# Kernel tuning notes

Hardware: AMD Instinct MI355X
Metric: run time of the kernel (lower is better)

Reference implementation:

```python
import jax, jax.numpy as jnp
import numpy as np

B, N, H, W = 128, 8192, 7, 7


def setup_inputs() -> dict:
    key = jax.random.key(0)
    ks = jax.random.split(key, 10)
    inp = {
        'x': jax.random.normal(ks[0], (B, N, H, W), dtype=jnp.float32),
        'y': jax.random.normal(ks[1], (B, N), dtype=jnp.float32),
        # nn.MultiheadAttention(embed_dim=1, num_heads=1) params (all scalar)
        'wq': jax.random.normal(ks[2], (), dtype=jnp.float32),
        'wk': jax.random.normal(ks[3], (), dtype=jnp.float32),
        'wv': jax.random.normal(ks[4], (), dtype=jnp.float32),
        'bq': jax.random.normal(ks[5], (), dtype=jnp.float32) * 0.1,
        'bk': jax.random.normal(ks[6], (), dtype=jnp.float32) * 0.1,
        'bv': jax.random.normal(ks[7], (), dtype=jnp.float32) * 0.1,
        'wo': jax.random.normal(ks[8], (), dtype=jnp.float32),
        'bo': jax.random.normal(ks[9], (), dtype=jnp.float32) * 0.1,
    }
    return inp


def _mha1(q_src, kv_src, wq, bq, wk, bk, wv, bv, wo, bo):
    # embed_dim=1, num_heads=1, scale = 1/sqrt(1) = 1.
    # torch sees (seq=B, batch=N, embed=1): attention mixes the B axis per n.
    q = q_src * wq + bq            # [B, N]
    k = kv_src * wk + bk           # [B, N]
    v = kv_src * wv + bv           # [B, N]
    scores = jnp.einsum('in,jn->ijn', q, k)      # [B, B, N]
    a = jax.nn.softmax(scores, axis=1)           # softmax over keys j
    out = jnp.einsum('ijn,jn->in', a, v)         # [B, N]
    return out * wo + bo


def reference(x, y, wq, bq, wk, bk, wv, bv, wo, bo):
    xp = jnp.mean(x, axis=(2, 3))                # AdaptiveAvgPool2d((1,1)) -> [B, N]
    self_x = _mha1(xp, xp, wq, bq, wk, bk, wv, bv, wo, bo)
    self_y = _mha1(y, y, wq, bq, wk, bk, wv, bv, wo, bo)
    cross_x = _mha1(xp, y, wq, bq, wk, bk, wv, bv, wo, bo)
    cross_y = _mha1(y, xp, wq, bq, wk, bk, wv, bv, wo, bo)
    f_x = xp + self_x
    f_y = y + self_y
    c_f_x = cross_x + f_x
    c_f_y = cross_y + f_y
    return jnp.concatenate((c_f_x, c_f_y), axis=1)   # [B, 2N]
```

## Files before the change

kernel.cpp:

```cpp
#include <hip/hip_runtime.h>


constexpr int B_SEQ = 128;
constexpr int N_COL = 8192;
constexpr int HWP   = 49;
constexpr int NT    = 256;
constexpr int TC    = 4;
constexpr int G     = 4;
constexpr int CPB   = TC * G;
constexpr int VSTR  = 132;
constexpr int OSTR  = 21;

typedef float v2f __attribute__((ext_vector_type(2)));

#if __has_builtin(__builtin_elementwise_fma)
#define VFMA(a, b, c) __builtin_elementwise_fma((a), (b), (c))
#else
__device__ __forceinline__ v2f VFMA(v2f a, v2f b, v2f c) {
    v2f r; r.x = fmaf(a.x, b.x, c.x); r.y = fmaf(a.y, b.y, c.y); return r;
}
#endif

__global__ __launch_bounds__(NT, 2) void rsca_fused(
    const float* __restrict__ x, const float* __restrict__ y,
    const float* __restrict__ pwq, const float* __restrict__ pwk,
    const float* __restrict__ pwv, const float* __restrict__ pbq,
    const float* __restrict__ pbk, const float* __restrict__ pbv,
    const float* __restrict__ pwo, const float* __restrict__ pbo,
    float* __restrict__ out)
{
    __shared__ float vls[2][2][TC * VSTR];
    __shared__ float pmn[2][2][8][TC];
    __shared__ float pmx[2][2][8][TC];
    __shared__ float obuf[2][B_SEQ * OSTR];

    const int t       = threadIdx.x;
    const int bid     = blockIdx.x;
    const int colbase = bid * CPB;
    const int ql      = t & 3;
    const int seg     = t >> 2;
    const int lane    = t & 63;
    const int wid     = t >> 6;

    const float wq = pwq[0], wk = pwk[0], wv = pwv[0];
    const float bq = pbq[0], bk = pbk[0], bv = pbv[0];
    const float wo = pwo[0], bo = pbo[0];
    const float L2E = 1.4426950408889634f;
    const float wkL = wk * L2E, bkL = bk * L2E;
    const float alpha = wo * wv;
    const float beta2 = 2.0f * (wo * bv + bo);

    auto issue_pass = [&](int g, int p, float4 (&v)[13]) {
        const int j = p * 64 + seg;
        const float4* __restrict__ base =
            (const float4*)(x + ((size_t)j * N_COL + colbase + g * TC) * (size_t)HWP);
        #pragma unroll
        for (int k = 0; k < 12; ++k) v[k] = base[ql + 4 * k];
        v[12] = base[48];
    };

    auto reduce_pass = [&](int p, int nb, const float4 (&v)[13]) {
        float s0 = 0.f, s1 = 0.f, s2 = 0.f, s3 = 0.f;
        s0 += v[0].x + v[0].y + v[0].z + v[0].w;
        s0 += v[1].x + v[1].y + v[1].z + v[1].w;
        s0 += v[2].x + v[2].y + v[2].z + v[2].w;
        s1 += v[4].x + v[4].y + v[4].z + v[4].w;
        s1 += v[5].x + v[5].y + v[5].z + v[5].w;
        s2 += v[7].x + v[7].y + v[7].z + v[7].w;
        s2 += v[8].x + v[8].y + v[8].z + v[8].w;
        s3 += v[10].x + v[10].y + v[10].z + v[10].w;
        s3 += v[11].x + v[11].y + v[11].z + v[11].w;
        { const float sm = v[3].x + v[3].y + v[3].z + v[3].w;
          const float cr = (ql == 0) ? v[3].x : 0.0f;
          s0 += cr; s1 += sm - cr; }
        { const float sm = v[6].x + v[6].y + v[6].z + v[6].w;
          const float cr = (ql == 0) ? (v[6].x + v[6].y) : 0.0f;
          s1 += cr; s2 += sm - cr; }
        { const float sm = v[9].x + v[9].y + v[9].z + v[9].w;
          const float cr = (ql == 0) ? (v[9].x + v[9].y + v[9].z) : 0.0f;
          s2 += cr; s3 += sm - cr; }
        const float tail = v[12].x + v[12].y + v[12].z + v[12].w;
        s0 += __shfl_xor(s0, 1); s1 += __shfl_xor(s1, 1);
        s2 += __shfl_xor(s2, 1); s3 += __shfl_xor(s3, 1);
        s0 += __shfl_xor(s0, 2); s1 += __shfl_xor(s1, 2);
        s2 += __shfl_xor(s2, 2); s3 += __shfl_xor(s3, 2);
        float r = s0;
        r = (ql == 1) ? s1 : r;
        r = (ql == 2) ? s2 : r;
        r = (ql == 3) ? (s3 + tail) : r;
        const float mean = r * (1.0f / HWP);
        const int j = p * 64 + seg;
        vls[nb][0][ql * VSTR + j] = mean;
        float mn = mean, mx = mean;
        #pragma unroll
        for (int off = 4; off <= 32; off <<= 1) {
            mn = fminf(mn, __shfl_xor(mn, off));
            mx = fmaxf(mx, __shfl_xor(mx, off));
        }
        if (lane < 4) {
            pmn[nb][0][p * 4 + wid][ql] = mn;
            pmx[nb][0][p * 4 + wid][ql] = mx;
        }
    };

    auto stage_y = [&](int nb, float fy0, float fy1) {
        vls[nb][1][ql * VSTR + seg]      = fy0;
        vls[nb][1][ql * VSTR + seg + 64] = fy1;
        float mn = fminf(fy0, fy1), mx = fmaxf(fy0, fy1);
        #pragma unroll
        for (int off = 4; off <= 32; off <<= 1) {
            mn = fminf(mn, __shfl_xor(mn, off));
            mx = fmaxf(mx, __shfl_xor(mx, off));
        }
        if (lane < 4) {
            pmn[nb][1][wid][ql] = mn;
            pmx[nb][1][wid][ql] = mx;
        }
    };

    const int ch = t >> 7;
    const int i  = t & (B_SEQ - 1);

    auto attn = [&](int g, int cb, int cc) {
        const int c = ch * 2 + cc;
        const float* __restrict__ vx = &vls[cb][0][c * VSTR];
        const float* __restrict__ vy = &vls[cb][1][c * VSTR];

        float vxmn = pmn[cb][0][0][c], vxmx = pmx[cb][0][0][c];
        #pragma unroll
        for (int s = 1; s < 8; ++s) {
            vxmn = fminf(vxmn, pmn[cb][0][s][c]);
            vxmx = fmaxf(vxmx, pmx[cb][0][s][c]);
        }
        float vymn = pmn[cb][1][0][c], vymx = pmx[cb][1][0][c];
        #pragma unroll
        for (int s = 1; s < 4; ++s) {
            vymn = fminf(vymn, pmn[cb][1][s][c]);
            vymx = fmaxf(vymx, pmx[cb][1][s][c]);
        }
        const float axv = fmaf(vxmx, wkL, bkL), bxv = fmaf(vxmn, wkL, bkL);
        const float kxmx = fmaxf(axv, bxv), kxmn = fminf(axv, bxv);
        const float ayv = fmaf(vymx, wkL, bkL), byv = fmaf(vymn, wkL, bkL);
        const float kymx = fmaxf(ayv, byv), kymn = fminf(ayv, byv);

        const float xi = vx[i], yi = vy[i];
        const float qx = fmaf(xi, wq, bq), qy = fmaf(yi, wq, bq);
        const float nmsx = -(qx >= 0.f ? qx * kxmx : qx * kxmn);
        const float nmcy = -(qy >= 0.f ? qy * kxmx : qy * kxmn);
        const float nmsy = -(qy >= 0.f ? qy * kymx : qy * kymn);
        const float nmcx = -(qx >= 0.f ? qx * kymx : qx * kymn);

        const float qxw = qx * wkL, qyw = qy * wkL;
        const v2f qxw2 = {qxw, qxw}, qyw2 = {qyw, qyw};
        const float csx = fmaf(qx, bkL, nmsx), ccy = fmaf(qy, bkL, nmcy);
        const float csy = fmaf(qy, bkL, nmsy), ccx = fmaf(qx, bkL, nmcx);
        const v2f csx2 = {csx, csx}, ccy2 = {ccy, ccy};
        const v2f csy2 = {csy, csy}, ccx2 = {ccx, ccx};

        v2f s0sx = {0.f, 0.f}, s1sx = {0.f, 0.f};
        v2f s0cy = {0.f, 0.f}, s1cy = {0.f, 0.f};
        v2f s0sy = {0.f, 0.f}, s1sy = {0.f, 0.f};
        v2f s0cx = {0.f, 0.f}, s1cx = {0.f, 0.f};

        for (int j0 = 0; j0 < B_SEQ; j0 += 8) {
            const float4 a0 = *(const float4*)&vx[j0];
            const float4 a1 = *(const float4*)&vx[j0 + 4];
            const float4 b0 = *(const float4*)&vy[j0];
            const float4 b1 = *(const float4*)&vy[j0 + 4];
            auto px2 = [&](float v0, float v1) {
                const v2f vv = {v0, v1};
                v2f t1 = VFMA(qxw2, vv, csx2);
                v2f e1; e1.x = __builtin_amdgcn_exp2f(t1.x);
                        e1.y = __builtin_amdgcn_exp2f(t1.y);
                s1sx = VFMA(e1, vv, s1sx); s0sx += e1;
                v2f t2 = VFMA(qyw2, vv, ccy2);
                v2f e2; e2.x = __builtin_amdgcn_exp2f(t2.x);
                        e2.y = __builtin_amdgcn_exp2f(t2.y);
                s1cy = VFMA(e2, vv, s1cy); s0cy += e2;
            };
            auto py2 = [&](float v0, float v1) {
                const v2f vv = {v0, v1};
                v2f t3 = VFMA(qyw2, vv, csy2);
                v2f e3; e3.x = __builtin_amdgcn_exp2f(t3.x);
                        e3.y = __builtin_amdgcn_exp2f(t3.y);
                s1sy = VFMA(e3, vv, s1sy); s0sy += e3;
                v2f t4 = VFMA(qxw2, vv, ccx2);
                v2f e4; e4.x = __builtin_amdgcn_exp2f(t4.x);
                        e4.y = __builtin_amdgcn_exp2f(t4.y);
                s1cx = VFMA(e4, vv, s1cx); s0cx += e4;
            };
            px2(a0.x, a0.y); px2(a0.z, a0.w); px2(a1.x, a1.y); px2(a1.z, a1.w);
            py2(b0.x, b0.y); py2(b0.z, b0.w); py2(b1.x, b1.y); py2(b1.z, b1.w);
        }
        const float S0sx = s0sx.x + s0sx.y, S1sx = s1sx.x + s1sx.y;
        const float S0cy = s0cy.x + s0cy.y, S1cy = s1cy.x + s1cy.y;
        const float S0sy = s0sy.x + s0sy.y, S1sy = s1sy.x + s1sy.y;
        const float S0cx = s0cx.x + s0cx.y, S1cx = s1cx.x + s1cx.y;
        const float mx_attn = S1sx * __builtin_amdgcn_rcpf(S0sx)
                            + S1cx * __builtin_amdgcn_rcpf(S0cx);
        const float my_attn = S1sy * __builtin_amdgcn_rcpf(S0sy)
                            + S1cy * __builtin_amdgcn_rcpf(S0cy);
        obuf[0][i * OSTR + g * TC + c] = fmaf(alpha, mx_attn, beta2 + xi);
        obuf[1][i * OSTR + g * TC + c] = fmaf(alpha, my_attn, beta2 + yi);
    };

    float4 va[13], vb[13];
    float fy0, fy1;
    {
        const int col = colbase + ql;
        issue_pass(0, 0, va);
        issue_pass(0, 1, vb);
        fy0 = y[(size_t)seg * N_COL + col];
        fy1 = y[(size_t)(seg + 64) * N_COL + col];
        reduce_pass(0, 0, va);
        stage_y(0, fy0, fy1);
        reduce_pass(1, 0, vb);
    }
    __syncthreads();

    int cur = 0;
    for (int g = 0; g < G; ++g) {
        const int nb = cur ^ 1;
        const bool pf = (g + 1 < G);
        if (pf) {
            const int col = colbase + (g + 1) * TC + ql;
            issue_pass(g + 1, 0, va);
            fy0 = y[(size_t)seg * N_COL + col];
            fy1 = y[(size_t)(seg + 64) * N_COL + col];
        }
        attn(g, cur, 0);
        if (pf) {
            reduce_pass(0, nb, va);
            stage_y(nb, fy0, fy1);
            issue_pass(g + 1, 1, vb);
        }
        attn(g, cur, 1);
        if (pf) reduce_pass(1, nb, vb);
        __syncthreads();
        cur = nb;
    }

    #pragma unroll
    for (int idx = t; idx < 2 * B_SEQ * TC; idx += NT) {
        const int set = idx >> 9;
        const int rem = idx & 511;
        const int ii  = rem >> 2;
        const int q   = rem & 3;
        const float* p = &obuf[set][ii * OSTR + q * 4];
        float4 val;
        val.x = p[0]; val.y = p[1]; val.z = p[2]; val.w = p[3];
        *(float4*)&out[(size_t)ii * (2 * N_COL) + (size_t)set * N_COL + colbase + q * 4] = val;
    }
}

extern "C" void kernel_launch(void* const* d_in, const int* in_sizes, int n_in,
                              void* d_out, int out_size, void* d_ws, size_t ws_size,
                              hipStream_t stream) {
    const float* x   = (const float*)d_in[0];
    const float* y   = (const float*)d_in[1];
    const float* pwq = (const float*)d_in[2];
    const float* pwk = (const float*)d_in[3];
    const float* pwv = (const float*)d_in[4];
    const float* pbq = (const float*)d_in[5];
    const float* pbk = (const float*)d_in[6];
    const float* pbv = (const float*)d_in[7];
    const float* pwo = (const float*)d_in[8];
    const float* pbo = (const float*)d_in[9];
    float* out = (float*)d_out;

    rsca_fused<<<dim3(N_COL / CPB), dim3(NT), 0, stream>>>(
        x, y, pwq, pwk, pwv, pbq, pbk, pbv, pwo, pbo, out);
}
```

Before: 326.5 us.

## Split fused kernel into pooling pass and separate attention kernel via workspace

Replaces the single fused pool+attention kernel with two kernels when a workspace is available. The first pools x into a transposed [N,B] buffer, and the second runs the attention with 512-thread blocks over 16 columns and a swizzled block-to-column mapping. The aim is to let the memory-bound pooling and the exp-bound attention each run with their own occupancy instead of being interleaved in one kernel. The cost is an extra global round trip for the pooled values and a second launch. The old fused path stays as a fallback when no workspace is given.

```diff
diff --git a/kernel.cpp b/kernel.cpp
--- a/kernel.cpp
+++ b/kernel.cpp
@@ -4,12 +4,6 @@
 constexpr int B_SEQ = 128;
 constexpr int N_COL = 8192;
 constexpr int HWP   = 49;
-constexpr int NT    = 256;
-constexpr int TC    = 4;
-constexpr int G     = 4;
-constexpr int CPB   = TC * G;
-constexpr int VSTR  = 132;
-constexpr int OSTR  = 21;
 
 typedef float v2f __attribute__((ext_vector_type(2)));
 
@@ -20,6 +14,227 @@
     v2f r; r.x = fmaf(a.x, b.x, c.x); r.y = fmaf(a.y, b.y, c.y); return r;
 }
 #endif
+
+constexpr int ANT = 256;
+constexpr int ATC = 4;
+
+__global__ __launch_bounds__(ANT, 6) void pool_x(
+    const float* __restrict__ x, float* __restrict__ xpT)
+{
+    const int t   = threadIdx.x;
+    const int n0  = blockIdx.x * ATC;
+    const int ql  = t & 3;
+    const int seg = t >> 2;
+
+    for (int pass = 0; pass < 2; ++pass) {
+        const int j = pass * 64 + seg;
+        const float4* __restrict__ base =
+            (const float4*)(x + ((size_t)j * N_COL + n0) * (size_t)HWP);
+        float4 v[13];
+        #pragma unroll
+        for (int k = 0; k < 12; ++k) v[k] = base[ql + 4 * k];
+        v[12] = base[48];
+
+        float s0 = 0.f, s1 = 0.f, s2 = 0.f, s3 = 0.f;
+        s0 += v[0].x + v[0].y + v[0].z + v[0].w;
+        s0 += v[1].x + v[1].y + v[1].z + v[1].w;
+        s0 += v[2].x + v[2].y + v[2].z + v[2].w;
+        s1 += v[4].x + v[4].y + v[4].z + v[4].w;
+        s1 += v[5].x + v[5].y + v[5].z + v[5].w;
+        s2 += v[7].x + v[7].y + v[7].z + v[7].w;
+        s2 += v[8].x + v[8].y + v[8].z + v[8].w;
+        s3 += v[10].x + v[10].y + v[10].z + v[10].w;
+        s3 += v[11].x + v[11].y + v[11].z + v[11].w;
+        { const float sm = v[3].x + v[3].y + v[3].z + v[3].w;
+          const float cr = (ql == 0) ? v[3].x : 0.0f;
+          s0 += cr; s1 += sm - cr; }
+        { const float sm = v[6].x + v[6].y + v[6].z + v[6].w;
+          const float cr = (ql == 0) ? (v[6].x + v[6].y) : 0.0f;
+          s1 += cr; s2 += sm - cr; }
+        { const float sm = v[9].x + v[9].y + v[9].z + v[9].w;
+          const float cr = (ql == 0) ? (v[9].x + v[9].y + v[9].z) : 0.0f;
+          s2 += cr; s3 += sm - cr; }
+        const float tail = v[12].x + v[12].y + v[12].z + v[12].w;
+
+        s0 += __shfl_xor(s0, 1); s1 += __shfl_xor(s1, 1);
+        s2 += __shfl_xor(s2, 1); s3 += __shfl_xor(s3, 1);
+        s0 += __shfl_xor(s0, 2); s1 += __shfl_xor(s1, 2);
+        s2 += __shfl_xor(s2, 2); s3 += __shfl_xor(s3, 2);
+        float r = s0;
+        r = (ql == 1) ? s1 : r;
+        r = (ql == 2) ? s2 : r;
+        r = (ql == 3) ? (s3 + tail) : r;
+        const float mean = r * (1.0f / HWP);
+        xpT[(size_t)(n0 + ql) * B_SEQ + j] = mean;
+    }
+}
+
+constexpr int BNT = 512;
+constexpr int BTC = 16;
+constexpr int OPAD = 17;
+
+__global__ __launch_bounds__(BNT, 4) void rsca_attn(
+    const float* __restrict__ xpT, const float* __restrict__ y,
+    const float* __restrict__ pwq, const float* __restrict__ pwk,
+    const float* __restrict__ pwv, const float* __restrict__ pbq,
+    const float* __restrict__ pbk, const float* __restrict__ pbv,
+    const float* __restrict__ pwo, const float* __restrict__ pbo,
+    float* __restrict__ out)
+{
+    __shared__ float xv[BTC][B_SEQ];
+    __shared__ float yv[BTC][B_SEQ];
+    __shared__ float pmny[8][BTC], pmxy[8][BTC];
+    __shared__ float pmnx[BTC], pmxx[BTC];
+    __shared__ float obuf[2][B_SEQ * OPAD];
+
+    const int t    = threadIdx.x;
+    const int lane = t & 63;
+    const int wv   = t >> 6;
+    const int cg = (blockIdx.x & 7) * ((int)gridDim.x >> 3) + (blockIdx.x >> 3);
+    const int n0 = cg * BTC;
+
+    const float wq = pwq[0], wk = pwk[0], wvv = pwv[0];
+    const float bq = pbq[0], bk = pbk[0], bv = pbv[0];
+    const float wo = pwo[0], bo = pbo[0];
+    const float L2E = 1.4426950408889634f;
+    const float wkL = wk * L2E, bkL = bk * L2E;
+    const float alpha = wo * wvv;
+    const float beta2 = 2.0f * (wo * bv + bo);
+
+    {
+        const float4 v4 = *(const float4*)&xpT[(size_t)n0 * B_SEQ + t * 4];
+        const int c  = t >> 5;
+        const int j0 = (t & 31) * 4;
+        *(float4*)&xv[c][j0] = v4;
+        float mn = fminf(fminf(v4.x, v4.y), fminf(v4.z, v4.w));
+        float mx = fmaxf(fmaxf(v4.x, v4.y), fmaxf(v4.z, v4.w));
+        #pragma unroll
+        for (int off = 1; off <= 16; off <<= 1) {
+            mn = fminf(mn, __shfl_xor(mn, off));
+            mx = fmaxf(mx, __shfl_xor(mx, off));
+        }
+        if ((lane & 31) == 0) { pmnx[c] = mn; pmxx[c] = mx; }
+    }
+    {
+        const int c  = t & 15;
+        const int jb = t >> 4;
+        float fy[4];
+        #pragma unroll
+        for (int r = 0; r < 4; ++r)
+            fy[r] = y[(size_t)(jb + 32 * r) * N_COL + n0 + c];
+        #pragma unroll
+        for (int r = 0; r < 4; ++r)
+            yv[c][jb + 32 * r] = fy[r];
+        float mn = fminf(fminf(fy[0], fy[1]), fminf(fy[2], fy[3]));
+        float mx = fmaxf(fmaxf(fy[0], fy[1]), fmaxf(fy[2], fy[3]));
+        mn = fminf(mn, __shfl_xor(mn, 16)); mx = fmaxf(mx, __shfl_xor(mx, 16));
+        mn = fminf(mn, __shfl_xor(mn, 32)); mx = fmaxf(mx, __shfl_xor(mx, 32));
+        if (lane < 16) { pmny[wv][c] = mn; pmxy[wv][c] = mx; }
+    }
+    __syncthreads();
+
+    const int ch = t >> 7;
+    const int i  = t & (B_SEQ - 1);
+
+    #pragma unroll
+    for (int cc = 0; cc < 4; ++cc) {
+        const int c = ch * 4 + cc;
+        const float* __restrict__ vx = xv[c];
+        const float* __restrict__ vy = yv[c];
+
+        const float vxmn = pmnx[c], vxmx = pmxx[c];
+        float vymn = pmny[0][c], vymx = pmxy[0][c];
+        #pragma unroll
+        for (int s = 1; s < 8; ++s) {
+            vymn = fminf(vymn, pmny[s][c]);
+            vymx = fmaxf(vymx, pmxy[s][c]);
+        }
+        const float axv = fmaf(vxmx, wkL, bkL), bxv = fmaf(vxmn, wkL, bkL);
+        const float kxmx = fmaxf(axv, bxv), kxmn = fminf(axv, bxv);
+        const float ayv = fmaf(vymx, wkL, bkL), byv = fmaf(vymn, wkL, bkL);
+        const float kymx = fmaxf(ayv, byv), kymn = fminf(ayv, byv);
+
+        const float xi = vx[i], yi = vy[i];
+        const float qx = fmaf(xi, wq, bq), qy = fmaf(yi, wq, bq);
+        const float nmsx = -(qx >= 0.f ? qx * kxmx : qx * kxmn);
+        const float nmcy = -(qy >= 0.f ? qy * kxmx : qy * kxmn);
+        const float nmsy = -(qy >= 0.f ? qy * kymx : qy * kymn);
+        const float nmcx = -(qx >= 0.f ? qx * kymx : qx * kymn);
+
+        const float qxw = qx * wkL, qyw = qy * wkL;
+        const v2f qxw2 = {qxw, qxw}, qyw2 = {qyw, qyw};
+        const float csx = fmaf(qx, bkL, nmsx), ccy = fmaf(qy, bkL, nmcy);
+        const float csy = fmaf(qy, bkL, nmsy), ccx = fmaf(qx, bkL, nmcx);
+        const v2f csx2 = {csx, csx}, ccy2 = {ccy, ccy};
+        const v2f csy2 = {csy, csy}, ccx2 = {ccx, ccx};
+
+        v2f s0sx = {0.f, 0.f}, s1sx = {0.f, 0.f};
+        v2f s0cy = {0.f, 0.f}, s1cy = {0.f, 0.f};
+        v2f s0sy = {0.f, 0.f}, s1sy = {0.f, 0.f};
+        v2f s0cx = {0.f, 0.f}, s1cx = {0.f, 0.f};
+
+        for (int j0 = 0; j0 < B_SEQ; j0 += 8) {
+            const float4 a0 = *(const float4*)&vx[j0];
+            const float4 a1 = *(const float4*)&vx[j0 + 4];
+            const float4 b0 = *(const float4*)&vy[j0];
+            const float4 b1 = *(const float4*)&vy[j0 + 4];
+            auto px2 = [&](float v0, float v1) {
+                const v2f vvj = {v0, v1};
+                v2f t1 = VFMA(qxw2, vvj, csx2);
+                v2f e1; e1.x = __builtin_amdgcn_exp2f(t1.x);
+                        e1.y = __builtin_amdgcn_exp2f(t1.y);
+                s1sx = VFMA(e1, vvj, s1sx); s0sx += e1;
+                v2f t2 = VFMA(qyw2, vvj, ccy2);
+                v2f e2; e2.x = __builtin_amdgcn_exp2f(t2.x);
+                        e2.y = __builtin_amdgcn_exp2f(t2.y);
+                s1cy = VFMA(e2, vvj, s1cy); s0cy += e2;
+            };
+            auto py2 = [&](float v0, float v1) {
+                const v2f vvj = {v0, v1};
+                v2f t3 = VFMA(qyw2, vvj, csy2);
+                v2f e3; e3.x = __builtin_amdgcn_exp2f(t3.x);
+                        e3.y = __builtin_amdgcn_exp2f(t3.y);
+                s1sy = VFMA(e3, vvj, s1sy); s0sy += e3;
+                v2f t4 = VFMA(qxw2, vvj, ccx2);
+                v2f e4; e4.x = __builtin_amdgcn_exp2f(t4.x);
+                        e4.y = __builtin_amdgcn_exp2f(t4.y);
+                s1cx = VFMA(e4, vvj, s1cx); s0cx += e4;
+            };
+            px2(a0.x, a0.y); px2(a0.z, a0.w); px2(a1.x, a1.y); px2(a1.z, a1.w);
+            py2(b0.x, b0.y); py2(b0.z, b0.w); py2(b1.x, b1.y); py2(b1.z, b1.w);
+        }
+        const float S0sx = s0sx.x + s0sx.y, S1sx = s1sx.x + s1sx.y;
+        const float S0cy = s0cy.x + s0cy.y, S1cy = s1cy.x + s1cy.y;
+        const float S0sy = s0sy.x + s0sy.y, S1sy = s1sy.x + s1sy.y;
+        const float S0cx = s0cx.x + s0cx.y, S1cx = s1cx.x + s1cx.y;
+        const float mx_attn = S1sx * __builtin_amdgcn_rcpf(S0sx)
+                            + S1cx * __builtin_amdgcn_rcpf(S0cx);
+        const float my_attn = S1sy * __builtin_amdgcn_rcpf(S0sy)
+                            + S1cy * __builtin_amdgcn_rcpf(S0cy);
+        obuf[0][i * OPAD + c] = fmaf(alpha, mx_attn, beta2 + xi);
+        obuf[1][i * OPAD + c] = fmaf(alpha, my_attn, beta2 + yi);
+    }
+    __syncthreads();
+
+    #pragma unroll
+    for (int k = 0; k < 2; ++k) {
+        const int fidx = t + k * BNT;
+        const int q   = fidx & 3;
+        const int ii  = (fidx >> 2) & (B_SEQ - 1);
+        const int set = fidx >> 9;
+        const float* p = &obuf[set][ii * OPAD + q * 4];
+        float4 val;
+        val.x = p[0]; val.y = p[1]; val.z = p[2]; val.w = p[3];
+        *(float4*)&out[(size_t)ii * (2 * N_COL) + (size_t)set * N_COL + n0 + q * 4] = val;
+    }
+}
+
+constexpr int NT  = 256;
+constexpr int TC  = 4;
+constexpr int G   = 4;
+constexpr int CPB = TC * G;
+constexpr int VSTR = 132;
+constexpr int OSTR = 21;
 
 __global__ __launch_bounds__(NT, 2) void rsca_fused(
     const float* __restrict__ x, const float* __restrict__ y,
@@ -123,8 +338,8 @@
 
     auto attn = [&](int g, int cb, int cc) {
         const int c = ch * 2 + cc;
-        const float* __restrict__ vx = &vls[cb][0][c * VSTR];
-        const float* __restrict__ vy = &vls[cb][1][c * VSTR];
+        const float* __restrict__ vx0 = &vls[cb][0][c * VSTR];
+        const float* __restrict__ vy0 = &vls[cb][1][c * VSTR];
 
         float vxmn = pmn[cb][0][0][c], vxmx = pmx[cb][0][0][c];
         #pragma unroll
@@ -143,7 +358,7 @@
         const float ayv = fmaf(vymx, wkL, bkL), byv = fmaf(vymn, wkL, bkL);
         const float kymx = fmaxf(ayv, byv), kymn = fminf(ayv, byv);
 
-        const float xi = vx[i], yi = vy[i];
+        const float xi = vx0[i], yi = vy0[i];
         const float qx = fmaf(xi, wq, bq), qy = fmaf(yi, wq, bq);
         const float nmsx = -(qx >= 0.f ? qx * kxmx : qx * kxmn);
         const float nmcy = -(qy >= 0.f ? qy * kxmx : qy * kxmn);
@@ -163,10 +378,10 @@
         v2f s0cx = {0.f, 0.f}, s1cx = {0.f, 0.f};
 
         for (int j0 = 0; j0 < B_SEQ; j0 += 8) {
-            const float4 a0 = *(const float4*)&vx[j0];
-            const float4 a1 = *(const float4*)&vx[j0 + 4];
-            const float4 b0 = *(const float4*)&vy[j0];
-            const float4 b1 = *(const float4*)&vy[j0 + 4];
+            const float4 a0 = *(const float4*)&vx0[j0];
+            const float4 a1 = *(const float4*)&vx0[j0 + 4];
+            const float4 b0 = *(const float4*)&vy0[j0];
+            const float4 b1 = *(const float4*)&vy0[j0 + 4];
             auto px2 = [&](float v0, float v1) {
                 const v2f vv = {v0, v1};
                 v2f t1 = VFMA(qxw2, vv, csx2);
@@ -268,6 +483,14 @@
     const float* pbo = (const float*)d_in[9];
     float* out = (float*)d_out;
 
-    rsca_fused<<<dim3(N_COL / CPB), dim3(NT), 0, stream>>>(
-        x, y, pwq, pwk, pwv, pbq, pbk, pbv, pwo, pbo, out);
+    const size_t need = (size_t)N_COL * B_SEQ * sizeof(float);
+    if (d_ws != nullptr && ws_size >= need) {
+        float* xpT = (float*)d_ws;
+        pool_x<<<dim3(N_COL / ATC), dim3(ANT), 0, stream>>>(x, xpT);
+        rsca_attn<<<dim3(N_COL / BTC), dim3(BNT), 0, stream>>>(
+            xpT, y, pwq, pwk, pwv, pbq, pbk, pbv, pwo, pbo, out);
+    } else {
+        rsca_fused<<<dim3(N_COL / CPB), dim3(NT), 0, stream>>>(
+            x, y, pwq, pwk, pwv, pbq, pbk, pbv, pwo, pbo, out);
+    }
 }
```

Measured after the change: 365.1 us. +11.8%, slower.

## Replace in-block double-buffered column groups with one 4-column group per block

Applied to the files above, without the earlier changes.

Each block now handles only 4 columns instead of 16, which removes the software-pipelined double-buffer loop and launches four times as many blocks. Launch bounds are raised to ask for more resident blocks per CU, and the blocks are remapped with an XCD-style swizzle of the block index. The attention inner loop also prefetches the next 8 shared-memory values one iteration ahead. The intent is to rely on occupancy across blocks rather than manual overlap to hide load latency. The cost is narrower output stores, extra per-block setup, and a tighter register budget.

```diff
diff --git a/kernel.cpp b/kernel.cpp
--- a/kernel.cpp
+++ b/kernel.cpp
@@ -6,10 +6,8 @@
 constexpr int HWP   = 49;
 constexpr int NT    = 256;
 constexpr int TC    = 4;
-constexpr int G     = 4;
-constexpr int CPB   = TC * G;
 constexpr int VSTR  = 132;
-constexpr int OSTR  = 21;
+constexpr int OSTR  = 5;
 
 typedef float v2f __attribute__((ext_vector_type(2)));
 
@@ -21,7 +19,7 @@
 }
 #endif
 
-__global__ __launch_bounds__(NT, 2) void rsca_fused(
+__global__ __launch_bounds__(NT, 5) void rsca_fused(
     const float* __restrict__ x, const float* __restrict__ y,
     const float* __restrict__ pwq, const float* __restrict__ pwk,
     const float* __restrict__ pwv, const float* __restrict__ pbq,
@@ -29,18 +27,21 @@
     const float* __restrict__ pwo, const float* __restrict__ pbo,
     float* __restrict__ out)
 {
-    __shared__ float vls[2][2][TC * VSTR];
-    __shared__ float pmn[2][2][8][TC];
-    __shared__ float pmx[2][2][8][TC];
+    __shared__ float xv[TC * VSTR];
+    __shared__ float yv[TC * VSTR];
+    __shared__ float pmnx[8][TC], pmxx[8][TC];
+    __shared__ float pmny[4][TC], pmxy[4][TC];
     __shared__ float obuf[2][B_SEQ * OSTR];
 
-    const int t       = threadIdx.x;
-    const int bid     = blockIdx.x;
-    const int colbase = bid * CPB;
-    const int ql      = t & 3;
-    const int seg     = t >> 2;
-    const int lane    = t & 63;
-    const int wid     = t >> 6;
+    const int t    = threadIdx.x;
+    const int bid  = blockIdx.x;
+    const int cg = (bid & 7) * ((N_COL / TC) >> 3) + (bid >> 3);
+    const int n0 = cg * TC;
+
+    const int ql   = t & 3;
+    const int seg  = t >> 2;
+    const int lane = t & 63;
+    const int wid  = t >> 6;
 
     const float wq = pwq[0], wk = pwk[0], wv = pwv[0];
     const float bq = pbq[0], bk = pbk[0], bv = pbv[0];
@@ -50,16 +51,30 @@
     const float alpha = wo * wv;
     const float beta2 = 2.0f * (wo * bv + bo);
 
-    auto issue_pass = [&](int g, int p, float4 (&v)[13]) {
-        const int j = p * 64 + seg;
+    {
+        const int j = t >> 2, c = t & 3;
+        const float fy0 = y[(size_t)j * N_COL + n0 + c];
+        const float fy1 = y[(size_t)(j + 64) * N_COL + n0 + c];
+        yv[c * VSTR + j]      = fy0;
+        yv[c * VSTR + j + 64] = fy1;
+        float mn = fminf(fy0, fy1), mx = fmaxf(fy0, fy1);
+        #pragma unroll
+        for (int off = 4; off <= 32; off <<= 1) {
+            mn = fminf(mn, __shfl_xor(mn, off));
+            mx = fmaxf(mx, __shfl_xor(mx, off));
+        }
+        if (lane < 4) { pmny[wid][lane] = mn; pmxy[wid][lane] = mx; }
+    }
+
+    for (int pass = 0; pass < 2; ++pass) {
+        const int j = pass * 64 + seg;
         const float4* __restrict__ base =
-            (const float4*)(x + ((size_t)j * N_COL + colbase + g * TC) * (size_t)HWP);
+            (const float4*)(x + ((size_t)j * N_COL + n0) * (size_t)HWP);
+        float4 v[13];
         #pragma unroll
         for (int k = 0; k < 12; ++k) v[k] = base[ql + 4 * k];
         v[12] = base[48];
-    };
-
-    auto reduce_pass = [&](int p, int nb, const float4 (&v)[13]) {
+
         float s0 = 0.f, s1 = 0.f, s2 = 0.f, s3 = 0.f;
         s0 += v[0].x + v[0].y + v[0].z + v[0].w;
         s0 += v[1].x + v[1].y + v[1].z + v[1].w;
@@ -80,6 +95,7 @@
           const float cr = (ql == 0) ? (v[9].x + v[9].y + v[9].z) : 0.0f;
           s2 += cr; s3 += sm - cr; }
         const float tail = v[12].x + v[12].y + v[12].z + v[12].w;
+
         s0 += __shfl_xor(s0, 1); s1 += __shfl_xor(s1, 1);
         s2 += __shfl_xor(s2, 1); s3 += __shfl_xor(s3, 1);
         s0 += __shfl_xor(s0, 2); s1 += __shfl_xor(s1, 2);
@@ -89,8 +105,8 @@
         r = (ql == 2) ? s2 : r;
         r = (ql == 3) ? (s3 + tail) : r;
         const float mean = r * (1.0f / HWP);
-        const int j = p * 64 + seg;
-        vls[nb][0][ql * VSTR + j] = mean;
+        xv[ql * VSTR + j] = mean;
+
         float mn = mean, mx = mean;
         #pragma unroll
         for (int off = 4; off <= 32; off <<= 1) {
@@ -98,45 +114,31 @@
             mx = fmaxf(mx, __shfl_xor(mx, off));
         }
         if (lane < 4) {
-            pmn[nb][0][p * 4 + wid][ql] = mn;
-            pmx[nb][0][p * 4 + wid][ql] = mx;
-        }
-    };
-
-    auto stage_y = [&](int nb, float fy0, float fy1) {
-        vls[nb][1][ql * VSTR + seg]      = fy0;
-        vls[nb][1][ql * VSTR + seg + 64] = fy1;
-        float mn = fminf(fy0, fy1), mx = fmaxf(fy0, fy1);
-        #pragma unroll
-        for (int off = 4; off <= 32; off <<= 1) {
-            mn = fminf(mn, __shfl_xor(mn, off));
-            mx = fmaxf(mx, __shfl_xor(mx, off));
-        }
-        if (lane < 4) {
-            pmn[nb][1][wid][ql] = mn;
-            pmx[nb][1][wid][ql] = mx;
-        }
-    };
-
+            pmnx[pass * 4 + wid][lane] = mn;
+            pmxx[pass * 4 + wid][lane] = mx;
+        }
+    }
+    __syncthreads();
+
+    const int i  = t & (B_SEQ - 1);
     const int ch = t >> 7;
-    const int i  = t & (B_SEQ - 1);
-
-    auto attn = [&](int g, int cb, int cc) {
+    #pragma unroll
+    for (int cc = 0; cc < 2; ++cc) {
         const int c = ch * 2 + cc;
-        const float* __restrict__ vx = &vls[cb][0][c * VSTR];
-        const float* __restrict__ vy = &vls[cb][1][c * VSTR];
-
-        float vxmn = pmn[cb][0][0][c], vxmx = pmx[cb][0][0][c];
+        const float* __restrict__ vx = &xv[c * VSTR];
+        const float* __restrict__ vy = &yv[c * VSTR];
+
+        float vxmn = pmnx[0][c], vxmx = pmxx[0][c];
         #pragma unroll
         for (int s = 1; s < 8; ++s) {
-            vxmn = fminf(vxmn, pmn[cb][0][s][c]);
-            vxmx = fmaxf(vxmx, pmx[cb][0][s][c]);
-        }
-        float vymn = pmn[cb][1][0][c], vymx = pmx[cb][1][0][c];
+            vxmn = fminf(vxmn, pmnx[s][c]);
+            vxmx = fmaxf(vxmx, pmxx[s][c]);
+        }
+        float vymn = pmny[0][c], vymx = pmxy[0][c];
         #pragma unroll
         for (int s = 1; s < 4; ++s) {
-            vymn = fminf(vymn, pmn[cb][1][s][c]);
-            vymx = fmaxf(vymx, pmx[cb][1][s][c]);
+            vymn = fminf(vymn, pmny[s][c]);
+            vymx = fmaxf(vymx, pmxy[s][c]);
         }
         const float axv = fmaf(vxmx, wkL, bkL), bxv = fmaf(vxmn, wkL, bkL);
         const float kxmx = fmaxf(axv, bxv), kxmn = fminf(axv, bxv);
@@ -162,35 +164,42 @@
         v2f s0sy = {0.f, 0.f}, s1sy = {0.f, 0.f};
         v2f s0cx = {0.f, 0.f}, s1cx = {0.f, 0.f};
 
+        auto px2 = [&](float v0, float v1) {
+            const v2f vvj = {v0, v1};
+            v2f t1 = VFMA(qxw2, vvj, csx2);
+            v2f e1; e1.x = __builtin_amdgcn_exp2f(t1.x);
+                    e1.y = __builtin_amdgcn_exp2f(t1.y);
+            s1sx = VFMA(e1, vvj, s1sx); s0sx += e1;
+            v2f t2 = VFMA(qyw2, vvj, ccy2);
+            v2f e2; e2.x = __builtin_amdgcn_exp2f(t2.x);
+                    e2.y = __builtin_amdgcn_exp2f(t2.y);
+            s1cy = VFMA(e2, vvj, s1cy); s0cy += e2;
+        };
+        auto py2 = [&](float v0, float v1) {
+            const v2f vvj = {v0, v1};
+            v2f t3 = VFMA(qyw2, vvj, csy2);
+            v2f e3; e3.x = __builtin_amdgcn_exp2f(t3.x);
+                    e3.y = __builtin_amdgcn_exp2f(t3.y);
+            s1sy = VFMA(e3, vvj, s1sy); s0sy += e3;
+            v2f t4 = VFMA(qxw2, vvj, ccx2);
+            v2f e4; e4.x = __builtin_amdgcn_exp2f(t4.x);
+                    e4.y = __builtin_amdgcn_exp2f(t4.y);
+            s1cx = VFMA(e4, vvj, s1cx); s0cx += e4;
+        };
+
+        float4 a0 = *(const float4*)&vx[0], a1 = *(const float4*)&vx[4];
+        float4 b0 = *(const float4*)&vy[0], b1 = *(const float4*)&vy[4];
         for (int j0 = 0; j0 < B_SEQ; j0 += 8) {
-            const float4 a0 = *(const float4*)&vx[j0];
-            const float4 a1 = *(const float4*)&vx[j0 + 4];
-            const float4 b0 = *(const float4*)&vy[j0];
-            const float4 b1 = *(const float4*)&vy[j0 + 4];
-            auto px2 = [&](float v0, float v1) {
-                const v2f vv = {v0, v1};
-                v2f t1 = VFMA(qxw2, vv, csx2);
-                v2f e1; e1.x = __builtin_amdgcn_exp2f(t1.x);
-                        e1.y = __builtin_amdgcn_exp2f(t1.y);
-                s1sx = VFMA(e1, vv, s1sx); s0sx += e1;
-                v2f t2 = VFMA(qyw2, vv, ccy2);
-                v2f e2; e2.x = __builtin_amdgcn_exp2f(t2.x);
-                        e2.y = __builtin_amdgcn_exp2f(t2.y);
-                s1cy = VFMA(e2, vv, s1cy); s0cy += e2;
-            };
-            auto py2 = [&](float v0, float v1) {
-                const v2f vv = {v0, v1};
-                v2f t3 = VFMA(qyw2, vv, csy2);
-                v2f e3; e3.x = __builtin_amdgcn_exp2f(t3.x);
-                        e3.y = __builtin_amdgcn_exp2f(t3.y);
-                s1sy = VFMA(e3, vv, s1sy); s0sy += e3;
-                v2f t4 = VFMA(qxw2, vv, ccx2);
-                v2f e4; e4.x = __builtin_amdgcn_exp2f(t4.x);
-                        e4.y = __builtin_amdgcn_exp2f(t4.y);
-                s1cx = VFMA(e4, vv, s1cx); s0cx += e4;
-            };
+            const int jn = (j0 + 8) & (B_SEQ - 1);
+            float4 na0 = *(const float4*)&vx[jn];
+            float4 na1 = *(const float4*)&vx[jn + 4];
+            float4 nb0 = *(const float4*)&vy[jn];
+            float4 nb1 = *(const float4*)&vy[jn + 4];
+
             px2(a0.x, a0.y); px2(a0.z, a0.w); px2(a1.x, a1.y); px2(a1.z, a1.w);
             py2(b0.x, b0.y); py2(b0.z, b0.w); py2(b1.x, b1.y); py2(b1.z, b1.w);
+
+            a0 = na0; a1 = na1; b0 = nb0; b1 = nb1;
         }
         const float S0sx = s0sx.x + s0sx.y, S1sx = s1sx.x + s1sx.y;
         const float S0cy = s0cy.x + s0cy.y, S1cy = s1cy.x + s1cy.y;
@@ -200,56 +209,18 @@
                             + S1cx * __builtin_amdgcn_rcpf(S0cx);
         const float my_attn = S1sy * __builtin_amdgcn_rcpf(S0sy)
                             + S1cy * __builtin_amdgcn_rcpf(S0cy);
-        obuf[0][i * OSTR + g * TC + c] = fmaf(alpha, mx_attn, beta2 + xi);
-        obuf[1][i * OSTR + g * TC + c] = fmaf(alpha, my_attn, beta2 + yi);
-    };
-
-    float4 va[13], vb[13];
-    float fy0, fy1;
+        obuf[0][i * OSTR + c] = fmaf(alpha, mx_attn, beta2 + xi);
+        obuf[1][i * OSTR + c] = fmaf(alpha, my_attn, beta2 + yi);
+    }
+    __syncthreads();
+
     {
-        const int col = colbase + ql;
-        issue_pass(0, 0, va);
-        issue_pass(0, 1, vb);
-        fy0 = y[(size_t)seg * N_COL + col];
-        fy1 = y[(size_t)(seg + 64) * N_COL + col];
-        reduce_pass(0, 0, va);
-        stage_y(0, fy0, fy1);
-        reduce_pass(1, 0, vb);
-    }
-    __syncthreads();
-
-    int cur = 0;
-    for (int g = 0; g < G; ++g) {
-        const int nb = cur ^ 1;
-        const bool pf = (g + 1 < G);
-        if (pf) {
-            const int col = colbase + (g + 1) * TC + ql;
-            issue_pass(g + 1, 0, va);
-            fy0 = y[(size_t)seg * N_COL + col];
-            fy1 = y[(size_t)(seg + 64) * N_COL + col];
-        }
-        attn(g, cur, 0);
-        if (pf) {
-            reduce_pass(0, nb, va);
-            stage_y(nb, fy0, fy1);
-            issue_pass(g + 1, 1, vb);
-        }
-        attn(g, cur, 1);
-        if (pf) reduce_pass(1, nb, vb);
-        __syncthreads();
-        cur = nb;
-    }
-
-    #pragma unroll
-    for (int idx = t; idx < 2 * B_SEQ * TC; idx += NT) {
-        const int set = idx >> 9;
-        const int rem = idx & 511;
-        const int ii  = rem >> 2;
-        const int q   = rem & 3;
-        const float* p = &obuf[set][ii * OSTR + q * 4];
+        const int set = t >> 7;
+        const int ii  = t & (B_SEQ - 1);
+        const float* p = &obuf[set][ii * OSTR];
         float4 val;
         val.x = p[0]; val.y = p[1]; val.z = p[2]; val.w = p[3];
-        *(float4*)&out[(size_t)ii * (2 * N_COL) + (size_t)set * N_COL + colbase + q * 4] = val;
+        *(float4*)&out[(size_t)ii * (2 * N_COL) + (size_t)set * N_COL + n0] = val;
     }
 }
 
@@ -268,6 +239,6 @@
     const float* pbo = (const float*)d_in[9];
     float* out = (float*)d_out;
 
-    rsca_fused<<<dim3(N_COL / CPB), dim3(NT), 0, stream>>>(
+    rsca_fused<<<dim3(N_COL / TC), dim3(NT), 0, stream>>>(
         x, y, pwq, pwk, pwv, pbq, pbk, pbv, pwo, pbo, out);
 }
```

After: 322.9 us. About the same (-1.1%).
